# Kernel optimization log

Measured on AMD Instinct MI355X. Metric: run time of the kernel, lower is better.

The kernel has to match this reference:

```python
import jax, jax.numpy as jnp
import numpy as np

B, S, HIDDEN = 1, 2048, 2048
HEADS, HEAD_DIM = 32, 128
EPS = 1e-5
THETA = 10000.0


def setup_inputs() -> dict:
    key = jax.random.key(0)
    k0, k1, k2 = jax.random.split(key, 3)
    hidden_states = jax.random.normal(k0, (B, S, HIDDEN), jnp.float32)
    positions = jnp.broadcast_to(jnp.arange(S, dtype=jnp.int32)[None, :], (B, S))
    qkv_w = jax.random.normal(k1, (3 * HEADS * HEAD_DIM, HIDDEN), jnp.float32) * 0.02
    q_norm_w = jnp.ones((HEAD_DIM,), jnp.float32)
    k_norm_w = jnp.ones((HEAD_DIM,), jnp.float32)
    o_proj_w = jax.random.normal(k2, (HIDDEN, HEADS * HEAD_DIM), jnp.float32) * 0.02
    return {"hidden_states": hidden_states, "positions": positions, "qkv_w": qkv_w,
            "q_norm_w": q_norm_w, "k_norm_w": k_norm_w, "o_proj_w": o_proj_w}


def _rmsnorm(x, w):
    # RMSNorm over last (head_dim) axis
    var = jnp.mean(x * x, axis=-1, keepdims=True)
    return x * jax.lax.rsqrt(var + EPS) * w


def _rope(x, positions):
    # NeoX-style (non-interleaved) rotary over full head_dim
    d2 = HEAD_DIM // 2
    inv_freq = 1.0 / (THETA ** (jnp.arange(0, HEAD_DIM, 2, dtype=jnp.float32) / HEAD_DIM))
    freqs = positions.astype(jnp.float32)[..., None] * inv_freq  # [B,S,d2]
    cos = jnp.cos(freqs)[:, :, None, :]  # [B,S,1,d2]
    sin = jnp.sin(freqs)[:, :, None, :]
    x1, x2 = x[..., :d2], x[..., d2:]
    return jnp.concatenate([x1 * cos - x2 * sin, x2 * cos + x1 * sin], axis=-1)


def reference(hidden_states, positions, qkv_w, q_norm_w, k_norm_w, o_proj_w):
    b, s, _ = hidden_states.shape
    qkv = jnp.einsum('bsh,oh->bso', hidden_states, qkv_w)  # [B,S,3*H*D]
    q, k, v = jnp.split(qkv, 3, axis=-1)
    q = q.reshape(b, s, HEADS, HEAD_DIM)
    k = k.reshape(b, s, HEADS, HEAD_DIM)
    v = v.reshape(b, s, HEADS, HEAD_DIM)
    # qk_norm (per-head RMSNorm)
    q = _rmsnorm(q, q_norm_w)
    k = _rmsnorm(k, k_norm_w)
    # rotary embedding
    q = _rope(q, positions)
    k = _rope(k, positions)
    # causal attention, scale = head_dim**-0.5 (flash_attn default)
    scale = HEAD_DIM ** -0.5
    scores = jnp.einsum('bqhd,bkhd->bhqk', q, k) * scale  # [B,H,S,S]
    causal = jnp.tril(jnp.ones((s, s), dtype=bool))
    scores = jnp.where(causal[None, None], scores, jnp.float32(-1e30))
    probs = jax.nn.softmax(scores, axis=-1)
    o = jnp.einsum('bhqk,bkhd->bqhd', probs, v).reshape(b, s, HEADS * HEAD_DIM)
    return jnp.einsum('bso,ho->bsh', o, o_proj_w)
```

## Files before the change

### kernel.cpp

```cpp
#include <hip/hip_runtime.h>
#include <cstdint>
#include <cstddef>

static constexpr int S_LEN = 2048;
static constexpr int HID   = 2048;
static constexpr int NH    = 32;
static constexpr int HD    = 128;
static constexpr int OD    = 4096;
static constexpr int QKV_O = 12288;

#define AS1 __attribute__((address_space(1)))
#define AS3 __attribute__((address_space(3)))

typedef __attribute__((ext_vector_type(8))) short bf16x8;
typedef __attribute__((ext_vector_type(4))) float f32x4;
typedef __attribute__((ext_vector_type(4))) short s16x4;

template <int V> struct IC { static constexpr int v = V; };

__device__ __forceinline__ short f2bf(float f) {
  unsigned u = __float_as_uint(f);
  unsigned r = (u + 0x7fffu + ((u >> 16) & 1u)) >> 16;
  return (short)r;
}
__device__ __forceinline__ float bf2f(short s) {
  return __uint_as_float(((unsigned)(unsigned short)s) << 16);
}
__device__ __forceinline__ unsigned pk2bf(float a, float b) {
  return __builtin_amdgcn_perm(__float_as_uint(b), __float_as_uint(a), 0x07060302u);
}

__global__ void convert2_kernel(const float* __restrict__ in1, short* __restrict__ out1, int n1_4,
                                const float* __restrict__ in2, short* __restrict__ out2, int n2_4) {
  int i = blockIdx.x * blockDim.x + threadIdx.x;
  const float* in; short* out; int j;
  if (i < n1_4) { in = in1; out = out1; j = i; }
  else { j = i - n1_4; if (j >= n2_4) return; in = in2; out = out2; }
  float4 f = ((const float4*)in)[j];
  s16x4 s;
  s.x = f2bf(f.x); s.y = f2bf(f.y); s.z = f2bf(f.z); s.w = f2bf(f.w);
  ((s16x4*)out)[j] = s;
}

template <int BNT, int CMODE>
__global__ __launch_bounds__(512, 2) void gemm8p(
    const short* __restrict__ A, const short* __restrict__ Bw, void* __restrict__ Cp,
    int K, int N, int ldc) {
  constexpr int BH  = BNT / 128;
  constexpr int NJ  = BNT / 64;
  constexpr int NJH = NJ / 2;
  __shared__ short Al[2][128 * 64];
  __shared__ short Bl[2][BH][128 * 64];
  const int tid  = threadIdx.x;
  const int lane = tid & 63;
  const int quad = lane >> 4;
  const int col  = lane & 15;
  const int wave = tid >> 6;
  const int wm   = wave >> 2;
  const int wn   = wave & 3;

  const int nbn = N / BNT;
  const int nbm = gridDim.x / nbn;
  const int xcd = blockIdx.x & 7;
  const int u   = blockIdx.x >> 3;
  const int m0  = (u % nbm) * 128;
  const int n0  = (xcd * (nbn >> 3) + u / nbm) * BNT;

  const int NT = K >> 6;

  f32x4 acc[4][NJ] = {};
  bf16x8 a[4][2], b0[NJH][2], b1[NJH][2];

  auto stA = [&](int t, int buf) {
#pragma unroll
    for (int r = 0; r < 2; ++r) {
      int idx = r * 512 + tid;
      int row = idx >> 3;
      int g   = idx & 7;
      int gs  = g ^ ((row >> 1) & 7);
      const short* ga = A + (size_t)(m0 + row) * K + t * 64 + gs * 8;
      __builtin_amdgcn_global_load_lds((const AS1 unsigned*)ga,
                                       (AS3 unsigned*)&Al[buf][idx * 8], 16, 0, 0);
    }
  };
  auto stB = [&](int t, int buf, int h) {
#pragma unroll
    for (int r = 0; r < 2; ++r) {
      int idx = r * 512 + tid;
      int row = idx >> 3;
      int g   = idx & 7;
      int gs  = g ^ ((row >> 1) & 7);
      const short* gb = Bw + (size_t)(n0 + h * 128 + row) * K + t * 64 + gs * 8;
      __builtin_amdgcn_global_load_lds((const AS1 unsigned*)gb,
                                       (AS3 unsigned*)&Bl[buf][h][idx * 8], 16, 0, 0);
    }
  };
  auto rdA = [&](int buf, int mh) {
#pragma unroll
    for (int i = 0; i < 2; ++i) {
      int rh = wm * 64 + (mh * 2 + i) * 16 + col;
#pragma unroll
      for (int kf = 0; kf < 2; ++kf)
        a[mh * 2 + i][kf] =
            *(const bf16x8*)&Al[buf][rh * 64 + (((kf * 4 + quad) ^ ((rh >> 1) & 7)) * 8)];
    }
  };
  auto rdB = [&](int buf, int nh, bf16x8 (&bb)[NJH][2]) {
#pragma unroll
    for (int j = 0; j < NJH; ++j) {
      int br = wn * (BNT / 4) + nh * (BNT / 8) + j * 16 + col;
      int bh = br >> 7, rh = br & 127;
#pragma unroll
      for (int kf = 0; kf < 2; ++kf)
        bb[j][kf] =
            *(const bf16x8*)&Bl[buf][bh][rh * 64 + (((kf * 4 + quad) ^ ((rh >> 1) & 7)) * 8)];
    }
  };
  auto mm = [&](auto MH, auto NHc, bf16x8 (&bb)[NJH][2]) {
    constexpr int mh = MH.v, nh = NHc.v;
    __builtin_amdgcn_s_setprio(1);
#pragma unroll
    for (int i = 0; i < 2; ++i)
#pragma unroll
      for (int j = 0; j < NJH; ++j)
#pragma unroll
        for (int kf = 0; kf < 2; ++kf)
          acc[mh * 2 + i][nh * NJH + j] = __builtin_amdgcn_mfma_f32_16x16x32_bf16(
              a[mh * 2 + i][kf], bb[j][kf], acc[mh * 2 + i][nh * NJH + j], 0, 0, 0);
    __builtin_amdgcn_s_setprio(0);
  };
#define LGK() do { asm volatile("s_waitcnt lgkmcnt(0)"); __builtin_amdgcn_sched_barrier(0); } while (0)
#define BAR() __builtin_amdgcn_s_barrier()
  auto vmc_mid = [] {
    if constexpr (BH == 1) asm volatile("s_waitcnt vmcnt(4)" ::: "memory");
    else                   asm volatile("s_waitcnt vmcnt(6)" ::: "memory");
  };
  auto vmc_end = [] {
    if constexpr (BH == 1)      asm volatile("s_waitcnt vmcnt(4)" ::: "memory");
    else if constexpr (BH == 2) asm volatile("s_waitcnt vmcnt(6)" ::: "memory");
    else                        asm volatile("s_waitcnt vmcnt(8)" ::: "memory");
  };

#pragma unroll
  for (int h = 0; h < BH; ++h) stB(0, 0, h);
  stA(0, 0);
#pragma unroll
  for (int h = 0; h < BH; ++h) stB(1, 1, h);
  stA(1, 1);
  if constexpr (BH == 1)      asm volatile("s_waitcnt vmcnt(4)" ::: "memory");
  else if constexpr (BH == 2) asm volatile("s_waitcnt vmcnt(6)" ::: "memory");
  else                        asm volatile("s_waitcnt vmcnt(8)" ::: "memory");
  BAR();

  for (int i = 0; i < (NT >> 1); ++i) {
    const int t  = 2 * i;
    const int tA = (t + 2 < NT) ? t + 2 : NT - 2;
    const int tB = (t + 3 < NT) ? t + 3 : NT - 1;
    rdA(0, 0); rdB(0, 0, b0);
    BAR(); LGK();
    mm(IC<0>{}, IC<0>{}, b0);
    BAR();
    rdB(0, 1, b1);
    BAR(); LGK();
    mm(IC<0>{}, IC<1>{}, b1);
    BAR();
    rdA(0, 1);
    stB(tA, 0, 0);
    BAR(); LGK();
    mm(IC<1>{}, IC<1>{}, b1);
    BAR();
    if constexpr (BH >= 2) stB(tA, 0, 1);
    stA(tA, 0);
    BAR();
    mm(IC<1>{}, IC<0>{}, b0);
    vmc_mid();
    BAR();
    rdA(1, 0); rdB(1, 0, b0);
    if constexpr (BH == 3) stB(tA, 0, 2);
    BAR(); LGK();
    mm(IC<0>{}, IC<0>{}, b0);
    BAR();
    rdB(1, 1, b1);
    BAR(); LGK();
    mm(IC<0>{}, IC<1>{}, b1);
    BAR();
    rdA(1, 1);
    stB(tB, 1, 0);
    if constexpr (BH >= 2) stB(tB, 1, 1);
    BAR(); LGK();
    mm(IC<1>{}, IC<1>{}, b1);
    BAR();
    if constexpr (BH == 3) stB(tB, 1, 2);
    stA(tB, 1);
    BAR();
    mm(IC<1>{}, IC<0>{}, b0);
    vmc_end();
    BAR();
  }
#undef LGK
#undef BAR

#pragma unroll
  for (int mi = 0; mi < 4; ++mi)
#pragma unroll
    for (int nj = 0; nj < NJ; ++nj)
#pragma unroll
      for (int r = 0; r < 4; ++r) {
        int rr = m0 + wm * 64 + mi * 16 + quad * 4 + r;
        int cc = n0 + wn * (BNT / 4) + nj * 16 + col;
        if (CMODE == 1)
          ((float*)Cp)[(size_t)rr * ldc + cc] = acc[mi][nj][r];
        else
          ((short*)Cp)[(size_t)rr * ldc + cc] = f2bf(acc[mi][nj][r]);
      }
}

#define BM 128
#define BK 32

template <int BNT, int CMODE>
__global__ __launch_bounds__(256, 2) void gemm_nt_f32w(
    const short* __restrict__ A, const float* __restrict__ B, void* __restrict__ Cp,
    int K, int ldc) {
  __shared__ short Alds[2][BM * BK];
  __shared__ short Blds[2][BNT * BK];
  constexpr int WN  = BNT / 2;
  constexpr int NJ  = WN / 16;
  constexpr int BCH = (BNT * 4) / 256;
  const int tid  = threadIdx.x;
  const int lane = tid & 63;
  const int quad = lane >> 4;
  const int col  = lane & 15;
  const int wave = tid >> 6;
  const int m0 = blockIdx.y * BM;
  const int n0 = blockIdx.x * BNT;
  const int wm = (wave & 1) * 64;
  const int wn = (wave >> 1) * WN;

  f32x4 acc[4][NJ] = {};
  float4 breg[BCH][2];

  const int nk = K / BK;

  auto b_issue = [&](int k0) {
#pragma unroll
    for (int it = 0; it < BCH; ++it) {
      int idx = it * 256 + tid;
      int row = idx >> 2;
      int c   = idx & 3;
      const float* gb = B + (size_t)(n0 + row) * K + k0 + c * 8;
      breg[it][0] = *(const float4*)gb;
      breg[it][1] = *(const float4*)(gb + 4);
    }
  };
  auto a_issue = [&](int k0, int buf) {
#pragma unroll
    for (int it = 0; it < 2; ++it) {
      int idx = it * 256 + tid;
      int row = idx >> 2;
      int c   = idx & 3;
      int cs  = c ^ ((row >> 1) & 3);
      const short* ga = A + (size_t)(m0 + row) * K + k0 + cs * 8;
      __builtin_amdgcn_global_load_lds((const AS1 unsigned*)ga,
                                       (AS3 unsigned*)&Alds[buf][idx * 8], 16, 0, 0);
    }
  };
  auto b_write = [&](int buf) {
#pragma unroll
    for (int it = 0; it < BCH; ++it) {
      int idx = it * 256 + tid;
      int row = idx >> 2;
      int c   = idx & 3;
      int cw  = c ^ ((row >> 1) & 3);
      union { unsigned u[4]; bf16x8 v; } pk;
      pk.u[0] = pk2bf(breg[it][0].x, breg[it][0].y);
      pk.u[1] = pk2bf(breg[it][0].z, breg[it][0].w);
      pk.u[2] = pk2bf(breg[it][1].x, breg[it][1].y);
      pk.u[3] = pk2bf(breg[it][1].z, breg[it][1].w);
      *(bf16x8*)&Blds[buf][(row * 4 + cw) * 8] = pk.v;
    }
  };
  auto compute = [&](int buf) {
    bf16x8 a[4], b[NJ];
#pragma unroll
    for (int i = 0; i < 4; ++i) {
      int row = wm + i * 16 + col;
      a[i] = *(const bf16x8*)&Alds[buf][(row * 4 + (quad ^ ((row >> 1) & 3))) * 8];
    }
#pragma unroll
    for (int j = 0; j < NJ; ++j) {
      int row = wn + j * 16 + col;
      b[j] = *(const bf16x8*)&Blds[buf][(row * 4 + (quad ^ ((row >> 1) & 3))) * 8];
    }
#pragma unroll
    for (int i = 0; i < 4; ++i)
#pragma unroll
      for (int j = 0; j < NJ; ++j)
        acc[i][j] = __builtin_amdgcn_mfma_f32_16x16x32_bf16(a[i], b[j], acc[i][j], 0, 0, 0);
  };

  b_issue(0);
  a_issue(0, 0);
  b_write(0);
  __syncthreads();

  for (int t = 0; t < nk - 1; ++t) {
    const int cur = t & 1;
    b_issue((t + 1) * BK);
    a_issue((t + 1) * BK, cur ^ 1);
    compute(cur);
    b_write(cur ^ 1);
    __syncthreads();
  }
  compute((nk - 1) & 1);

#pragma unroll
  for (int i = 0; i < 4; ++i)
#pragma unroll
    for (int j = 0; j < NJ; ++j)
#pragma unroll
      for (int r = 0; r < 4; ++r) {
        int rr = m0 + wm + i * 16 + quad * 4 + r;
        int cc = n0 + wn + j * 16 + col;
        if (CMODE == 1)
          ((float*)Cp)[(size_t)rr * ldc + cc] = acc[i][j][r];
        else
          ((short*)Cp)[(size_t)rr * ldc + cc] = f2bf(acc[i][j][r]);
      }
}

__global__ void normrope_packv_kernel(short* __restrict__ qkv,
                                      const int* __restrict__ positions,
                                      const float* __restrict__ qw,
                                      const float* __restrict__ kw,
                                      short* __restrict__ vtp) {
  __shared__ short T[64][136];
  if (blockIdx.x < 32768) {
    int item = blockIdx.x * 4 + (threadIdx.x >> 6);
    int lane = threadIdx.x & 63;
    int head  = item & 31;
    int which = (item >> 5) & 1;
    int s     = item >> 6;
    const float* w = which ? kw : qw;
    short* base = qkv + (size_t)s * QKV_O + which * OD + head * HD;

    float x1 = bf2f(base[lane]);
    float x2 = bf2f(base[lane + 64]);
    float ss = x1 * x1 + x2 * x2;
#pragma unroll
    for (int d = 32; d; d >>= 1) ss += __shfl_xor(ss, d);
    float r = rsqrtf(ss * (1.0f / 128.0f) + 1e-5f);
    float xn1 = x1 * r * w[lane];
    float xn2 = x2 * r * w[lane + 64];

    float pos = (float)positions[s];
    float inv_freq = exp2f((float)lane * (-13.287712379549449f / 64.0f));
    float f = pos * inv_freq;
    float c = cosf(f), sn = sinf(f);
    float sc = which ? 1.0f : 0.12751863738f;
    base[lane]      = f2bf((xn1 * c - xn2 * sn) * sc);
    base[lane + 64] = f2bf((xn2 * c + xn1 * sn) * sc);
  } else {
    int bid2 = blockIdx.x - 32768;
    const int h  = bid2 & 31;
    const int kt = bid2 >> 5;
    const int tid = threadIdx.x;
    {
      int rr = tid >> 2;
      int db = (tid & 3) * 32;
      const short* src = qkv + (size_t)(kt * 64 + rr) * QKV_O + 2 * OD + h * HD + db;
#pragma unroll
      for (int i = 0; i < 4; ++i)
        *(bf16x8*)&T[rr][db + i * 8] = *(const bf16x8*)(src + i * 8);
    }
    __syncthreads();
    {
      int d  = tid >> 1;
      int k0 = (tid & 1) * 32;
      short* dst = vtp + (((size_t)h * 32 + kt) * 128 + d) * 64 + k0;
#pragma unroll
      for (int c = 0; c < 4; ++c) {
        bf16x8 v;
#pragma unroll
        for (int j = 0; j < 8; ++j) v[j] = T[k0 + c * 8 + j][d];
        *(bf16x8*)&dst[c * 8] = v;
      }
    }
  }
}

__global__ __launch_bounds__(256, 3) void attn_kernel(
    const short* __restrict__ qkv, const short* __restrict__ vtp, short* __restrict__ obuf) {
  __shared__ short Klds[64 * 128];
  __shared__ short Vt[128 * 64];
  __shared__ short Plds[4][16 * 64];

  const int tid  = threadIdx.x;
  const int lane = tid & 63;
  const int wave = tid >> 6;
  const int quad = lane >> 4;
  const int col  = lane & 15;
  const int h    = blockIdx.y;

  const int kr  = tid >> 2;
  const int kcb = (tid & 3) * 32;
  const int vd  = tid >> 1;
  const int vcb = (tid & 1) * 32;

  bf16x8 kreg[4], vreg[4];

  auto loadK = [&](int kt) {
    const short* kp = qkv + (size_t)(kt * 64 + kr) * QKV_O + OD + h * HD + kcb;
#pragma unroll
    for (int i = 0; i < 4; ++i) kreg[i] = *(const bf16x8*)(kp + i * 8);
  };
  auto loadV = [&](int kt) {
    const short* vp = vtp + (((size_t)h * 32 + kt) * 128 + vd) * 64 + vcb;
#pragma unroll
    for (int i = 0; i < 4; ++i) vreg[i] = *(const bf16x8*)(vp + i * 8);
  };
  auto writeKV = [&]() {
#pragma unroll
    for (int i = 0; i < 4; ++i) {
      int swz = ((tid & 3) * 4 + i) ^ (kr & 15);
      *(bf16x8*)&Klds[kr * 128 + swz * 8] = kreg[i];
    }
#pragma unroll
    for (int i = 0; i < 4; ++i) {
      int swz = ((tid & 1) * 4 + i) ^ (vd & 7);
      *(bf16x8*)&Vt[vd * 64 + swz * 8] = vreg[i];
    }
  };

#pragma unroll 1
  for (int half = 0; half < 2; ++half) {
    const int qt = half == 0 ? blockIdx.x : 31 - blockIdx.x;
    const int qbase = qt * 64 + wave * 16;

    bf16x8 qf[4];
#pragma unroll
    for (int kf = 0; kf < 4; ++kf)
      qf[kf] = *(const bf16x8*)(qkv + (size_t)(qbase + col) * QKV_O + h * HD + kf * 32 + quad * 8);

    f32x4 o[8] = {};
    float m_r[4], l_i[4];
#pragma unroll
    for (int r = 0; r < 4; ++r) { m_r[r] = -1e30f; l_i[r] = 0.f; }

    loadK(0); loadV(0);

#pragma unroll 1
    for (int kt = 0; kt <= qt; ++kt) {
      __syncthreads();
      writeKV();
      __syncthreads();
      if (kt < qt) { loadK(kt + 1); loadV(kt + 1); }

      f32x4 sfr[4];
      __builtin_amdgcn_s_setprio(1);
#pragma unroll
      for (int nf = 0; nf < 4; ++nf) {
        f32x4 acc = {};
#pragma unroll
        for (int kf = 0; kf < 4; ++kf) {
          bf16x8 b = *(const bf16x8*)&Klds[(nf * 16 + col) * 128 + ((kf * 4 + quad) ^ col) * 8];
          acc = __builtin_amdgcn_mfma_f32_16x16x32_bf16(qf[kf], b, acc, 0, 0, 0);
        }
        sfr[nf] = acc;
      }
      __builtin_amdgcn_s_setprio(0);

      if (kt == qt) {
#pragma unroll
        for (int nf = 0; nf < 4; ++nf)
#pragma unroll
          for (int r = 0; r < 4; ++r) {
            int key = kt * 64 + nf * 16 + col;
            int qg  = qbase + quad * 4 + r;
            if (key > qg) sfr[nf][r] = -1e30f;
          }
      }

#pragma unroll
      for (int r = 0; r < 4; ++r) {
        float mt = fmaxf(fmaxf(sfr[0][r], sfr[1][r]), fmaxf(sfr[2][r], sfr[3][r]));
#pragma unroll
        for (int d = 8; d; d >>= 1) mt = fmaxf(mt, __shfl_xor(mt, d));
        float mnew = fmaxf(m_r[r], mt);
        bool defer = __all(mnew - m_r[r] <= 8.0f);
        if (defer) mnew = m_r[r];
        float alpha = exp2f(m_r[r] - mnew);
        float ps = 0.f;
#pragma unroll
        for (int nf = 0; nf < 4; ++nf) {
          float p = exp2f(sfr[nf][r] - mnew);
          sfr[nf][r] = p;
          ps += p;
        }
        l_i[r] = l_i[r] * alpha + ps;
        if (!defer) {
#pragma unroll
          for (int nf = 0; nf < 8; ++nf) o[nf][r] *= alpha;
          m_r[r] = mnew;
        }
      }

#pragma unroll
      for (int nf = 0; nf < 4; ++nf)
#pragma unroll
        for (int r = 0; r < 4; ++r) {
          int row = quad * 4 + r;
          int key = nf * 16 + col;
          Plds[wave][row * 64 + ((key >> 3) ^ (row & 7)) * 8 + (key & 7)] = f2bf(sfr[nf][r]);
        }

      bf16x8 pa[2];
#pragma unroll
      for (int kf = 0; kf < 2; ++kf)
        pa[kf] = *(const bf16x8*)&Plds[wave][col * 64 + ((kf * 4 + quad) ^ (col & 7)) * 8];
      __builtin_amdgcn_s_setprio(1);
#pragma unroll
      for (int nf = 0; nf < 8; ++nf)
#pragma unroll
        for (int kf = 0; kf < 2; ++kf) {
          bf16x8 vb = *(const bf16x8*)&Vt[(nf * 16 + col) * 64 + ((kf * 4 + quad) ^ (col & 7)) * 8];
          o[nf] = __builtin_amdgcn_mfma_f32_16x16x32_bf16(pa[kf], vb, o[nf], 0, 0, 0);
        }
      __builtin_amdgcn_s_setprio(0);
    }

#pragma unroll
    for (int r = 0; r < 4; ++r) {
      float lt = l_i[r];
#pragma unroll
      for (int d = 8; d; d >>= 1) lt += __shfl_xor(lt, d);
      float inv = 1.0f / lt;
      int sg = qbase + quad * 4 + r;
#pragma unroll
      for (int nf = 0; nf < 8; ++nf)
        obuf[(size_t)sg * OD + h * HD + nf * 16 + col] = f2bf(o[nf][r] * inv);
    }
  }
}

extern "C" void kernel_launch(void* const* d_in, const int* in_sizes, int n_in,
                              void* d_out, int out_size, void* d_ws, size_t ws_size,
                              hipStream_t stream) {
  (void)in_sizes; (void)n_in; (void)out_size;
  const float* hs   = (const float*)d_in[0];
  const int*   pos  = (const int*)d_in[1];
  const float* qkvw = (const float*)d_in[2];
  const float* qw   = (const float*)d_in[3];
  const float* kw   = (const float*)d_in[4];
  const float* ow   = (const float*)d_in[5];
  float* out = (float*)d_out;

  char* ws = (char*)d_ws;
  short* qkvb    = (short*)(ws);
  short* obuf    = (short*)(ws + 50331648);
  short* qkvw_bf = (short*)(ws + 67108864);
  short* ow_bf   = (short*)(ws + 67108864);
  short* hsb  = (short*)d_out;
  short* vtp  = (short*)d_out;

  const bool fast = ws_size >= (size_t)117440512;

  if (fast) {
    int n1 = (S_LEN * HID) / 4, n2 = (QKV_O * HID) / 4;
    convert2_kernel<<<(n1 + n2 + 255) / 256, 256, 0, stream>>>(hs, hsb, n1, qkvw, qkvw_bf, n2);
    gemm8p<256, 0><<<(S_LEN / 128) * (QKV_O / 256), 512, 0, stream>>>(
        hsb, qkvw_bf, qkvb, HID, QKV_O, QKV_O);
    int n3 = (HID * OD) / 4;
    convert2_kernel<<<(n3 + 255) / 256, 256, 0, stream>>>(ow, ow_bf, n3, ow, ow_bf, 0);
  } else {
    int n1 = (S_LEN * HID) / 4;
    convert2_kernel<<<(n1 + 255) / 256, 256, 0, stream>>>(hs, hsb, n1, hs, hsb, 0);
    gemm_nt_f32w<128, 0><<<dim3(QKV_O / 128, S_LEN / BM), 256, 0, stream>>>(
        hsb, qkvw, qkvb, HID, QKV_O);
  }

  normrope_packv_kernel<<<(S_LEN * 2 * NH) / 4 + NH * (S_LEN / 64), 256, 0, stream>>>(
      qkvb, pos, qw, kw, vtp);

  attn_kernel<<<dim3(16, NH), 256, 0, stream>>>(qkvb, vtp, obuf);

  if (fast) {
    gemm8p<128, 1><<<(S_LEN / 128) * (HID / 128), 512, 0, stream>>>(
        obuf, ow_bf, out, OD, HID, HID);
  } else {
    gemm_nt_f32w<64, 1><<<dim3(HID / 64, S_LEN / BM), 256, 0, stream>>>(
        obuf, ow, out, OD, HID);
  }
}
```

Before: 490.7 us.

## Restructure GEMM to 4-phase pipeline and double-buffer K/V in attention

```diff
diff --git a/kernel.cpp b/kernel.cpp
--- a/kernel.cpp
+++ b/kernel.cpp
@@ -43,12 +43,11 @@
 }
 
 template <int BNT, int CMODE>
-__global__ __launch_bounds__(512, 2) void gemm8p(
+__global__ __launch_bounds__(512, 2) void gemm4p(
     const short* __restrict__ A, const short* __restrict__ Bw, void* __restrict__ Cp,
     int K, int N, int ldc) {
   constexpr int BH  = BNT / 128;
   constexpr int NJ  = BNT / 64;
-  constexpr int NJH = NJ / 2;
   __shared__ short Al[2][128 * 64];
   __shared__ short Bl[2][BH][128 * 64];
   const int tid  = threadIdx.x;
@@ -69,7 +68,7 @@
   const int NT = K >> 6;
 
   f32x4 acc[4][NJ] = {};
-  bf16x8 a[4][2], b0[NJH][2], b1[NJH][2];
+  bf16x8 a[2][2], b[NJ][2];
 
   auto stA = [&](int t, int buf) {
 #pragma unroll
@@ -83,17 +82,19 @@
                                        (AS3 unsigned*)&Al[buf][idx * 8], 16, 0, 0);
     }
   };
-  auto stB = [&](int t, int buf, int h) {
-#pragma unroll
-    for (int r = 0; r < 2; ++r) {
-      int idx = r * 512 + tid;
-      int row = idx >> 3;
-      int g   = idx & 7;
-      int gs  = g ^ ((row >> 1) & 7);
-      const short* gb = Bw + (size_t)(n0 + h * 128 + row) * K + t * 64 + gs * 8;
-      __builtin_amdgcn_global_load_lds((const AS1 unsigned*)gb,
-                                       (AS3 unsigned*)&Bl[buf][h][idx * 8], 16, 0, 0);
-    }
+  auto stB = [&](int t, int buf) {
+#pragma unroll
+    for (int h = 0; h < BH; ++h)
+#pragma unroll
+      for (int r = 0; r < 2; ++r) {
+        int idx = r * 512 + tid;
+        int row = idx >> 3;
+        int g   = idx & 7;
+        int gs  = g ^ ((row >> 1) & 7);
+        const short* gb = Bw + (size_t)(n0 + h * 128 + row) * K + t * 64 + gs * 8;
+        __builtin_amdgcn_global_load_lds((const AS1 unsigned*)gb,
+                                         (AS3 unsigned*)&Bl[buf][h][idx * 8], 16, 0, 0);
+      }
   };
   auto rdA = [&](int buf, int mh) {
 #pragma unroll
@@ -101,100 +102,72 @@
       int rh = wm * 64 + (mh * 2 + i) * 16 + col;
 #pragma unroll
       for (int kf = 0; kf < 2; ++kf)
-        a[mh * 2 + i][kf] =
+        a[i][kf] =
             *(const bf16x8*)&Al[buf][rh * 64 + (((kf * 4 + quad) ^ ((rh >> 1) & 7)) * 8)];
     }
   };
-  auto rdB = [&](int buf, int nh, bf16x8 (&bb)[NJH][2]) {
-#pragma unroll
-    for (int j = 0; j < NJH; ++j) {
-      int br = wn * (BNT / 4) + nh * (BNT / 8) + j * 16 + col;
+  auto rdB = [&](int buf) {
+#pragma unroll
+    for (int j = 0; j < NJ; ++j) {
+      int br = wn * (BNT / 4) + j * 16 + col;
       int bh = br >> 7, rh = br & 127;
 #pragma unroll
       for (int kf = 0; kf < 2; ++kf)
-        bb[j][kf] =
+        b[j][kf] =
             *(const bf16x8*)&Bl[buf][bh][rh * 64 + (((kf * 4 + quad) ^ ((rh >> 1) & 7)) * 8)];
     }
   };
-  auto mm = [&](auto MH, auto NHc, bf16x8 (&bb)[NJH][2]) {
-    constexpr int mh = MH.v, nh = NHc.v;
+  auto mm = [&](auto MH) {
+    constexpr int mh = MH.v;
     __builtin_amdgcn_s_setprio(1);
 #pragma unroll
     for (int i = 0; i < 2; ++i)
 #pragma unroll
-      for (int j = 0; j < NJH; ++j)
+      for (int j = 0; j < NJ; ++j)
 #pragma unroll
         for (int kf = 0; kf < 2; ++kf)
-          acc[mh * 2 + i][nh * NJH + j] = __builtin_amdgcn_mfma_f32_16x16x32_bf16(
-              a[mh * 2 + i][kf], bb[j][kf], acc[mh * 2 + i][nh * NJH + j], 0, 0, 0);
+          acc[mh * 2 + i][j] = __builtin_amdgcn_mfma_f32_16x16x32_bf16(
+              a[i][kf], b[j][kf], acc[mh * 2 + i][j], 0, 0, 0);
     __builtin_amdgcn_s_setprio(0);
   };
 #define LGK() do { asm volatile("s_waitcnt lgkmcnt(0)"); __builtin_amdgcn_sched_barrier(0); } while (0)
 #define BAR() __builtin_amdgcn_s_barrier()
-  auto vmc_mid = [] {
-    if constexpr (BH == 1) asm volatile("s_waitcnt vmcnt(4)" ::: "memory");
-    else                   asm volatile("s_waitcnt vmcnt(6)" ::: "memory");
-  };
-  auto vmc_end = [] {
-    if constexpr (BH == 1)      asm volatile("s_waitcnt vmcnt(4)" ::: "memory");
-    else if constexpr (BH == 2) asm volatile("s_waitcnt vmcnt(6)" ::: "memory");
-    else                        asm volatile("s_waitcnt vmcnt(8)" ::: "memory");
-  };
-
-#pragma unroll
-  for (int h = 0; h < BH; ++h) stB(0, 0, h);
+  auto vmc = [] {
+    if constexpr (BH == 2) asm volatile("s_waitcnt vmcnt(4)" ::: "memory");
+    else                   asm volatile("s_waitcnt vmcnt(2)" ::: "memory");
+  };
+
+  stB(0, 0);
   stA(0, 0);
-#pragma unroll
-  for (int h = 0; h < BH; ++h) stB(1, 1, h);
-  stA(1, 1);
-  if constexpr (BH == 1)      asm volatile("s_waitcnt vmcnt(4)" ::: "memory");
-  else if constexpr (BH == 2) asm volatile("s_waitcnt vmcnt(6)" ::: "memory");
-  else                        asm volatile("s_waitcnt vmcnt(8)" ::: "memory");
+  stB(1, 1);
+  vmc();
   BAR();
 
   for (int i = 0; i < (NT >> 1); ++i) {
     const int t  = 2 * i;
     const int tA = (t + 2 < NT) ? t + 2 : NT - 2;
     const int tB = (t + 3 < NT) ? t + 3 : NT - 1;
-    rdA(0, 0); rdB(0, 0, b0);
+    rdA(0, 0); rdB(0);
+    stA(t + 1, 1);
     BAR(); LGK();
-    mm(IC<0>{}, IC<0>{}, b0);
-    BAR();
-    rdB(0, 1, b1);
-    BAR(); LGK();
-    mm(IC<0>{}, IC<1>{}, b1);
+    mm(IC<0>{});
     BAR();
     rdA(0, 1);
-    stB(tA, 0, 0);
+    stB(tA, 0);
     BAR(); LGK();
-    mm(IC<1>{}, IC<1>{}, b1);
+    mm(IC<1>{});
+    vmc();
     BAR();
-    if constexpr (BH >= 2) stB(tA, 0, 1);
+    rdA(1, 0); rdB(1);
     stA(tA, 0);
-    BAR();
-    mm(IC<1>{}, IC<0>{}, b0);
-    vmc_mid();
-    BAR();
-    rdA(1, 0); rdB(1, 0, b0);
-    if constexpr (BH == 3) stB(tA, 0, 2);
     BAR(); LGK();
-    mm(IC<0>{}, IC<0>{}, b0);
-    BAR();
-    rdB(1, 1, b1);
-    BAR(); LGK();
-    mm(IC<0>{}, IC<1>{}, b1);
+    mm(IC<0>{});
     BAR();
     rdA(1, 1);
-    stB(tB, 1, 0);
-    if constexpr (BH >= 2) stB(tB, 1, 1);
+    stB(tB, 1);
     BAR(); LGK();
-    mm(IC<1>{}, IC<1>{}, b1);
-    BAR();
-    if constexpr (BH == 3) stB(tB, 1, 2);
-    stA(tB, 1);
-    BAR();
-    mm(IC<1>{}, IC<0>{}, b0);
-    vmc_end();
+    mm(IC<1>{});
+    vmc();
     BAR();
   }
 #undef LGK
@@ -389,10 +362,10 @@
   }
 }
 
-__global__ __launch_bounds__(256, 3) void attn_kernel(
+__global__ __launch_bounds__(256, 2) void attn_kernel(
     const short* __restrict__ qkv, const short* __restrict__ vtp, short* __restrict__ obuf) {
-  __shared__ short Klds[64 * 128];
-  __shared__ short Vt[128 * 64];
+  __shared__ short Klds[2][64 * 128];
+  __shared__ short Vt[2][128 * 64];
   __shared__ short Plds[4][16 * 64];
 
   const int tid  = threadIdx.x;
@@ -419,16 +392,16 @@
 #pragma unroll
     for (int i = 0; i < 4; ++i) vreg[i] = *(const bf16x8*)(vp + i * 8);
   };
-  auto writeKV = [&]() {
+  auto writeKV = [&](int buf) {
 #pragma unroll
     for (int i = 0; i < 4; ++i) {
       int swz = ((tid & 3) * 4 + i) ^ (kr & 15);
-      *(bf16x8*)&Klds[kr * 128 + swz * 8] = kreg[i];
+      *(bf16x8*)&Klds[buf][kr * 128 + swz * 8] = kreg[i];
     }
 #pragma unroll
     for (int i = 0; i < 4; ++i) {
       int swz = ((tid & 1) * 4 + i) ^ (vd & 7);
-      *(bf16x8*)&Vt[vd * 64 + swz * 8] = vreg[i];
+      *(bf16x8*)&Vt[buf][vd * 64 + swz * 8] = vreg[i];
     }
   };
 
@@ -448,13 +421,14 @@
     for (int r = 0; r < 4; ++r) { m_r[r] = -1e30f; l_i[r] = 0.f; }
 
     loadK(0); loadV(0);
+    __syncthreads();
+    writeKV(0);
 
 #pragma unroll 1
     for (int kt = 0; kt <= qt; ++kt) {
+      const int cur = kt & 1;
+      if (kt < qt) { loadK(kt + 1); loadV(kt + 1); }
       __syncthreads();
-      writeKV();
-      __syncthreads();
-      if (kt < qt) { loadK(kt + 1); loadV(kt + 1); }
 
       f32x4 sfr[4];
       __builtin_amdgcn_s_setprio(1);
@@ -463,7 +437,7 @@
         f32x4 acc = {};
 #pragma unroll
         for (int kf = 0; kf < 4; ++kf) {
-          bf16x8 b = *(const bf16x8*)&Klds[(nf * 16 + col) * 128 + ((kf * 4 + quad) ^ col) * 8];
+          bf16x8 b = *(const bf16x8*)&Klds[cur][(nf * 16 + col) * 128 + ((kf * 4 + quad) ^ col) * 8];
           acc = __builtin_amdgcn_mfma_f32_16x16x32_bf16(qf[kf], b, acc, 0, 0, 0);
         }
         sfr[nf] = acc;
@@ -523,10 +497,12 @@
       for (int nf = 0; nf < 8; ++nf)
 #pragma unroll
         for (int kf = 0; kf < 2; ++kf) {
-          bf16x8 vb = *(const bf16x8*)&Vt[(nf * 16 + col) * 64 + ((kf * 4 + quad) ^ (col & 7)) * 8];
+          bf16x8 vb = *(const bf16x8*)&Vt[cur][(nf * 16 + col) * 64 + ((kf * 4 + quad) ^ (col & 7)) * 8];
           o[nf] = __builtin_amdgcn_mfma_f32_16x16x32_bf16(pa[kf], vb, o[nf], 0, 0, 0);
         }
       __builtin_amdgcn_s_setprio(0);
+
+      if (kt < qt) writeKV(cur ^ 1);
     }
 
 #pragma unroll
@@ -568,7 +544,7 @@
   if (fast) {
     int n1 = (S_LEN * HID) / 4, n2 = (QKV_O * HID) / 4;
     convert2_kernel<<<(n1 + n2 + 255) / 256, 256, 0, stream>>>(hs, hsb, n1, qkvw, qkvw_bf, n2);
-    gemm8p<256, 0><<<(S_LEN / 128) * (QKV_O / 256), 512, 0, stream>>>(
+    gemm4p<256, 0><<<(S_LEN / 128) * (QKV_O / 256), 512, 0, stream>>>(
         hsb, qkvw_bf, qkvb, HID, QKV_O, QKV_O);
     int n3 = (HID * OD) / 4;
     convert2_kernel<<<(n3 + 255) / 256, 256, 0, stream>>>(ow, ow_bf, n3, ow, ow_bf, 0);
@@ -585,7 +561,7 @@
   attn_kernel<<<dim3(16, NH), 256, 0, stream>>>(qkvb, vtp, obuf);
 
   if (fast) {
-    gemm8p<128, 1><<<(S_LEN / 128) * (HID / 128), 512, 0, stream>>>(
+    gemm4p<128, 1><<<(S_LEN / 128) * (HID / 128), 512, 0, stream>>>(
         obuf, ow_bf, out, OD, HID, HID);
   } else {
     gemm_nt_f32w<64, 1><<<dim3(HID / 64, S_LEN / BM), 256, 0, stream>>>(
```

New measurement: 491.2 us. About the same (+0.1%).
